# Kernel tuning notes

Measured on AMD Instinct MI355X. Metric: run time of the kernel, lower is better.

The kernel has to match this reference:

```python
import jax, jax.numpy as jnp
import numpy as np

H = W = 224
NUM_COLS = 1024          # static padded ring width (>= max pixels in any radial ring, ~703)
SHUFFLE_FRACTION = 0.5
BATCH = 128

def _build_maps():
    centre = (H // 2, W // 2)
    Y, X = np.ogrid[:H, :W]
    dist = np.round(np.sqrt((X - centre[0]) ** 2 + (Y - centre[1]) ** 2)).astype(np.int32)
    num_rows = int(dist[0, 0]) + 1
    ax2 = np.zeros_like(dist)
    for d in range(num_rows):
        m = dist == d
        ax2[m] = np.arange(m.sum(), dtype=np.int32)  # row-major order within each ring
    return dist, ax2, num_rows

_DIST_NP, _AX2_NP, NUM_ROWS = _build_maps()
DIST_FLAT = jnp.asarray(_DIST_NP.reshape(-1))  # (H*W,) radial bin of each pixel
AX2_FLAT = jnp.asarray(_AX2_NP.reshape(-1))    # (H*W,) index within its ring

def _process_one(img, mrand, prand):
    # img: (H, W); mrand: (H, W); prand: (NUM_ROWS, NUM_COLS)
    sel = mrand < SHUFFLE_FRACTION
    masked = jnp.where(sel, img, jnp.nan)
    # scatter selected pixels into polar bins (pixel -> (dist, ax2) is a bijection)
    polar = jnp.full((NUM_ROWS, NUM_COLS), jnp.nan, dtype=img.dtype)
    polar = polar.at[DIST_FLAT, AX2_FLAT].set(masked.reshape(-1))
    # random per-row permutation of columns
    perm = jnp.argsort(prand, axis=1)
    shuf = jnp.take_along_axis(polar, perm, axis=1)
    # compact the non-NaN shuffled values (in column order) back into the
    # originally-occupied columns (in ascending order) -- same as the TF
    # argsort(dists)/boolean-mask scatter, expressed with static shapes.
    src_order = jnp.argsort(jnp.isnan(shuf), axis=1)    # stable: non-NaN cols first
    vals = jnp.take_along_axis(shuf, src_order, axis=1)
    dst_order = jnp.argsort(jnp.isnan(polar), axis=1)   # stable: occupied cols first
    rows = jnp.arange(NUM_ROWS)[:, None]
    reinserted = shuf.at[rows, dst_order].set(vals)
    # gather each pixel's (possibly shuffled) value and write back selected pixels
    new_vals = reinserted[DIST_FLAT, AX2_FLAT].reshape(H, W)
    return jnp.where(sel, new_vals, img)

def setup_inputs() -> dict:
    key = jax.random.key(0)
    k1, k2, k3 = jax.random.split(key, 3)
    images = jax.random.normal(k1, (BATCH, H, W, 1), dtype=jnp.float32)
    mask_rand = jax.random.uniform(k2, (BATCH, H, W), dtype=jnp.float32)
    perm_rand = jax.random.uniform(k3, (BATCH, NUM_ROWS, NUM_COLS), dtype=jnp.float32)
    return {"images": images, "mask_rand": mask_rand, "perm_rand": perm_rand}

def reference(images, mask_rand, perm_rand):
    out = jax.vmap(_process_one)(images[..., 0], mask_rand, perm_rand)
    return out[..., None]
```

## Files before the change

kernel.cpp:

```cpp
#include <hip/hip_runtime.h>

#define IMG_H 224
#define IMG_W 224
#define HW (IMG_H * IMG_W)
#define HWB (HW / 8)
#define NUM_ROWS 159
#define NUM_COLS 1024
#define BATCH 128
#define OVF_CAP 4096
#define MAXC 12
#define NBUCK 512
#define NHWORDS (NBUCK / 2)
#define WPL (NHWORDS / 64)

__device__ __forceinline__ int isqrt_i(int v) {
    int u = (int)sqrtf((float)v);
    while (u > 0 && u * u > v) --u;
    while ((u + 1) * (u + 1) <= v) ++u;
    return u;
}

__device__ __forceinline__ void lds_fence() {
    asm volatile("s_waitcnt lgkmcnt(0)" ::: "memory");
}

__global__ __launch_bounds__(256) void build_rings(unsigned short* __restrict__ ring_pix,
                                                   int* __restrict__ ring_cnt,
                                                   int* __restrict__ ovf_cnt) {
    const int d = blockIdx.x;
    const int tid = threadIdx.x;
    __shared__ int scnt[256];
    if (d == 0 && tid == 0) ovf_cnt[0] = 0;

    int cnt = 0;
    int x0l = 0, x1l = -1, x0r = 0, x1r = -1;
    if (tid < IMG_H) {
        const int dy = tid - 112;
        const int Araw = (d == 0) ? 0 : (d * d - d + 1);
        int A = Araw - dy * dy;
        if (A < 0) A = 0;
        const int B = d * d + d - dy * dy;
        if (B >= 0) {
            const int hi = isqrt_i(B);
            int lo = isqrt_i(A);
            if (lo * lo < A) ++lo;
            if (lo <= hi) {
                if (lo == 0) {
                    x0l = 112 - min(hi, 112);
                    x1l = 112 + min(hi, 111);
                } else {
                    x0l = 112 - min(hi, 112);
                    x1l = 112 - lo;
                    x0r = 112 + lo;
                    x1r = 112 + min(hi, 111);
                }
                cnt = max(0, x1l - x0l + 1) + max(0, x1r - x0r + 1);
            }
        }
    }
    scnt[tid] = cnt;
    __syncthreads();
    for (int off = 1; off < 256; off <<= 1) {
        const int mine = scnt[tid];
        const int add = (tid >= off) ? scnt[tid - off] : 0;
        __syncthreads();
        scnt[tid] = mine + add;
        __syncthreads();
    }
    if (tid < IMG_H && cnt > 0) {
        int j = d * NUM_COLS + (scnt[tid] - cnt);
        const int rowbase = tid * IMG_W;
        for (int x = x0l; x <= x1l; ++x) ring_pix[j++] = (unsigned short)(rowbase + x);
        for (int x = x0r; x <= x1r; ++x) ring_pix[j++] = (unsigned short)(rowbase + x);
    }
    if (tid == 255) ring_cnt[d] = scnt[255];
}

__global__ __launch_bounds__(256) void copy_sel(const float4* __restrict__ img4,
                                                const float4* __restrict__ mask4,
                                                float4* __restrict__ out4,
                                                unsigned char* __restrict__ selb) {
    const int t = blockIdx.x * 256 + threadIdx.x;
    const float4 i0 = img4[2 * t];
    const float4 i1 = img4[2 * t + 1];
    const float4 m0 = mask4[2 * t];
    const float4 m1 = mask4[2 * t + 1];
    out4[2 * t] = i0;
    out4[2 * t + 1] = i1;
    const unsigned by = (m0.x < 0.5f ? 1u : 0u) | (m0.y < 0.5f ? 2u : 0u) |
                        (m0.z < 0.5f ? 4u : 0u) | (m0.w < 0.5f ? 8u : 0u) |
                        (m1.x < 0.5f ? 16u : 0u) | (m1.y < 0.5f ? 32u : 0u) |
                        (m1.z < 0.5f ? 64u : 0u) | (m1.w < 0.5f ? 128u : 0u);
    selb[t] = (unsigned char)by;
}

__device__ __forceinline__ void sort_run(unsigned long long* __restrict__ srt,
                                         int s, int e) {
    for (int i = s + 1; i < e; ++i) {
        const unsigned long long key = srt[i];
        int j = i - 1;
        while (j >= s && srt[j] > key) {
            srt[j + 1] = srt[j];
            --j;
        }
        srt[j + 1] = key;
    }
}

template <int CAP>
__device__ int gather_count_sort(
    int b, int d, int lane,
    const float* __restrict__ img, const unsigned char* __restrict__ selb,
    const float* __restrict__ prand, float* __restrict__ out,
    const unsigned short* __restrict__ ring_pix, int n,
    unsigned long long* __restrict__ srt, unsigned* __restrict__ hist,
    unsigned short* __restrict__ dstpix, float* __restrict__ vlds) {
    const float* imgb = img + (size_t)b * HW;
    const unsigned char* sbb = selb + (size_t)b * HWB;
    const float* prb = prand + ((size_t)b * NUM_ROWS + d) * NUM_COLS;
    float* outb = out + (size_t)b * HW;
    const unsigned long long ltmask = (1ull << lane) - 1ull;
    const unsigned short* rp = ring_pix + d * NUM_COLS;

#pragma unroll
    for (int t = 0; t < WPL; ++t) hist[t * 64 + lane] = 0;

    int p[MAXC];
    unsigned char sb[MAXC];
    unsigned kb[MAXC];
#pragma unroll
    for (int c = 0; c < MAXC; ++c) p[c] = rp[min(c * 64 + lane, n - 1)];
#pragma unroll
    for (int c = 0; c < MAXC; ++c) sb[c] = sbb[p[c] >> 3];
#pragma unroll
    for (int c = 0; c < MAXC; ++c) kb[c] = __float_as_uint(prb[min(c * 64 + lane, n - 1)]);

    unsigned selm = 0;
#pragma unroll
    for (int c = 0; c < MAXC; ++c) {
        const int i = c * 64 + lane;
        if ((i < n) && ((sb[c] >> (p[c] & 7)) & 1)) selm |= 1u << c;
    }

    float v[MAXC];
#pragma unroll
    for (int c = 0; c < MAXC; ++c)
        if ((selm >> c) & 1) v[c] = imgb[p[c]];

    lds_fence();

    int base = 0;
#pragma unroll
    for (int c = 0; c < MAXC; ++c) {
        const bool sel = (selm >> c) & 1;
        const unsigned long long ball = __ballot(sel);
        if (sel) {
            const int j = base + __popcll(ball & ltmask);
            if (j < CAP) dstpix[j] = (unsigned short)p[c];
            const int bk = (int)(__uint_as_float(kb[c]) * (float)NBUCK);
            atomicAdd(&hist[bk >> 1], 1u << ((bk & 1) * 16));
        }
        base += __popcll(ball);
    }
    const int base_static = base;
    for (int c0 = MAXC * 64; c0 < n; c0 += 64) {
        const int i = c0 + lane;
        bool sel = false;
        int pp = 0;
        unsigned kk = 0;
        if (i < n) {
            pp = rp[i];
            kk = __float_as_uint(prb[i]);
            sel = (sbb[pp >> 3] >> (pp & 7)) & 1;
        }
        const unsigned long long ball = __ballot(sel);
        if (sel) {
            const int j = base + __popcll(ball & ltmask);
            if (j < CAP) {
                dstpix[j] = (unsigned short)pp;
                vlds[j] = imgb[pp];
            }
            const int bk = (int)(__uint_as_float(kk) * (float)NBUCK);
            atomicAdd(&hist[bk >> 1], 1u << ((bk & 1) * 16));
        }
        base += __popcll(ball);
    }
    const int k = base;
    if (k > CAP) return k;
    if (k == 0) return 0;

    lds_fence();

    unsigned neww[WPL];
    unsigned run = 0;
#pragma unroll
    for (int t = 0; t < WPL; ++t) {
        const unsigned w = hist[lane * WPL + t];
        const unsigned c0 = w & 0xffffu;
        neww[t] = run | ((run + c0) << 16);
        run += c0 + (w >> 16);
    }
    const unsigned own = run;
#pragma unroll
    for (int off = 1; off < 64; off <<= 1) {
        const unsigned o = __shfl_up(run, off, 64);
        if (lane >= off) run += o;
    }
    const unsigned bx = run - own;
    const unsigned bxp = bx | (bx << 16);
    unsigned st[WPL];
#pragma unroll
    for (int t = 0; t < WPL; ++t) {
        st[t] = neww[t] + bxp;
        hist[lane * WPL + t] = st[t];
    }

    lds_fence();

    int jb = 0;
#pragma unroll
    for (int c = 0; c < MAXC; ++c) {
        const bool sel = (selm >> c) & 1;
        const unsigned long long ball = __ballot(sel);
        if (sel) {
            const int j = jb + __popcll(ball & ltmask);
            const int bk = (int)(__uint_as_float(kb[c]) * (float)NBUCK);
            const unsigned sh = (unsigned)((bk & 1) * 16);
            const unsigned old = atomicAdd(&hist[bk >> 1], 1u << sh);
            const int pos = (int)((old >> sh) & 0xffffu);
            srt[pos] = ((unsigned long long)kb[c] << 16) | (unsigned)j;
            vlds[j] = v[c];
        }
        jb += __popcll(ball);
    }
    int tb = base_static;
    for (int c0 = MAXC * 64; c0 < n; c0 += 64) {
        const int i = c0 + lane;
        bool sel = false;
        int pp = 0;
        unsigned kk = 0;
        if (i < n) {
            pp = rp[i];
            kk = __float_as_uint(prb[i]);
            sel = (sbb[pp >> 3] >> (pp & 7)) & 1;
        }
        const unsigned long long ball = __ballot(sel);
        if (sel) {
            const int j = tb + __popcll(ball & ltmask);
            const int bk = (int)(__uint_as_float(kk) * (float)NBUCK);
            const unsigned sh = (unsigned)((bk & 1) * 16);
            const unsigned old = atomicAdd(&hist[bk >> 1], 1u << sh);
            const int pos = (int)((old >> sh) & 0xffffu);
            srt[pos] = ((unsigned long long)kk << 16) | (unsigned)j;
        }
        tb += __popcll(ball);
    }

    lds_fence();

#pragma unroll
    for (int t = 0; t < WPL; ++t) {
        const unsigned wend = hist[lane * WPL + t];
        const unsigned ws0 = st[t];
        sort_run(srt, (int)(ws0 & 0xffffu), (int)(wend & 0xffffu));
        sort_run(srt, (int)(ws0 >> 16), (int)(wend >> 16));
    }

    lds_fence();

    const unsigned short* s16 = (const unsigned short*)srt;
#pragma unroll
    for (int e = 0; e < CAP / 64; ++e) {
        const int r = e * 64 + lane;
        if (r < k) {
            const int j = s16[4 * r];
            const float val = vlds[j];
            outb[dstpix[r]] = val;
        }
    }
    return k;
}

__global__ __launch_bounds__(256) void radial_shuffle(
    const float* __restrict__ img, const unsigned char* __restrict__ selb,
    const float* __restrict__ prand, float* __restrict__ out,
    const unsigned short* __restrict__ ring_pix, const int* __restrict__ ring_cnt,
    int* __restrict__ ovf_cnt, int* __restrict__ ovf_list) {
    const int tid = threadIdx.x;
    const int wid = tid >> 6;
    const int lane = tid & 63;
    const int xcd = blockIdx.x & 7;
    const int g = (blockIdx.x >> 3) * 4 + wid;
    const int b = xcd * (BATCH / 8) + g / NUM_ROWS;
    const int d = g % NUM_ROWS;
    const int n = ring_cnt[d];

    __shared__ unsigned long long srt_s[4][512];
    __shared__ unsigned hist_s[4][NHWORDS];
    __shared__ unsigned short dp_s[4][512];
    __shared__ float vl_s[4][512];

    const int k = gather_count_sort<512>(b, d, lane, img, selb, prand, out,
                                         ring_pix, n, srt_s[wid], hist_s[wid],
                                         dp_s[wid], vl_s[wid]);

    if (k > 512) {
        if (lane == 0) {
            const int idx = atomicAdd(ovf_cnt, 1);
            if (idx < OVF_CAP) ovf_list[idx] = b * NUM_ROWS + d;
        }
    }
}

__global__ __launch_bounds__(64) void overflow_sort(
    const float* __restrict__ img, const unsigned char* __restrict__ selb,
    const float* __restrict__ prand, float* __restrict__ out,
    const unsigned short* __restrict__ ring_pix, const int* __restrict__ ring_cnt,
    const int* __restrict__ ovf_cnt, const int* __restrict__ ovf_list) {
    __shared__ unsigned long long srt[1024];
    __shared__ unsigned hist[NHWORDS];
    __shared__ unsigned short dstpix[1024];
    __shared__ float vlds[1024];
    const int m = min(*ovf_cnt, OVF_CAP);
    const int lane = threadIdx.x;
    for (int t = blockIdx.x; t < m; t += gridDim.x) {
        const int bd = ovf_list[t];
        const int b = bd / NUM_ROWS;
        const int d = bd % NUM_ROWS;
        gather_count_sort<1024>(b, d, lane, img, selb, prand, out, ring_pix,
                                ring_cnt[d], srt, hist, dstpix, vlds);
        __syncthreads();
    }
}

extern "C" void kernel_launch(void* const* d_in, const int* in_sizes, int n_in,
                              void* d_out, int out_size, void* d_ws, size_t ws_size,
                              hipStream_t stream) {
    const float* img   = (const float*)d_in[0];
    const float* mask  = (const float*)d_in[1];
    const float* prand = (const float*)d_in[2];
    float* out = (float*)d_out;

    unsigned short* ring_pix = (unsigned short*)d_ws;
    int* ring_cnt = (int*)((char*)d_ws + NUM_ROWS * NUM_COLS * sizeof(unsigned short));
    int* ovf_cnt  = ring_cnt + NUM_ROWS;
    int* ovf_list = ovf_cnt + 1;
    unsigned char* selb = (unsigned char*)(ovf_list + OVF_CAP);

    hipLaunchKernelGGL(build_rings, dim3(NUM_ROWS), dim3(256), 0, stream,
                       ring_pix, ring_cnt, ovf_cnt);
    hipLaunchKernelGGL(copy_sel, dim3(BATCH * HW / 8 / 256), dim3(256), 0, stream,
                       (const float4*)img, (const float4*)mask, (float4*)out, selb);
    hipLaunchKernelGGL(radial_shuffle, dim3(BATCH * NUM_ROWS / 4), dim3(256), 0,
                       stream, img, selb, prand, out, ring_pix, ring_cnt,
                       ovf_cnt, ovf_list);
    hipLaunchKernelGGL(overflow_sort, dim3(32), dim3(64), 0, stream,
                       img, selb, prand, out, ring_pix, ring_cnt,
                       ovf_cnt, ovf_list);
}
```

Baseline: 201.0 us.

## Fuse pre-pass kernels, split sort keys, and scatter outputs directly per pixel

After: 198.4 us. Within noise of the previous version (-1.3%).

```diff
diff --git a/kernel.cpp b/kernel.cpp
--- a/kernel.cpp
+++ b/kernel.cpp
@@ -24,97 +24,101 @@
     asm volatile("s_waitcnt lgkmcnt(0)" ::: "memory");
 }
 
-__global__ __launch_bounds__(256) void build_rings(unsigned short* __restrict__ ring_pix,
-                                                   int* __restrict__ ring_cnt,
-                                                   int* __restrict__ ovf_cnt) {
-    const int d = blockIdx.x;
+__global__ __launch_bounds__(256) void pre_pass(
+    const float4* __restrict__ img4, const float4* __restrict__ mask4,
+    float4* __restrict__ out4, unsigned char* __restrict__ selb,
+    unsigned short* __restrict__ ring_pix, int* __restrict__ ring_cnt,
+    int* __restrict__ ovf_cnt) {
+    const int bid = blockIdx.x;
     const int tid = threadIdx.x;
     __shared__ int scnt[256];
-    if (d == 0 && tid == 0) ovf_cnt[0] = 0;
-
-    int cnt = 0;
-    int x0l = 0, x1l = -1, x0r = 0, x1r = -1;
-    if (tid < IMG_H) {
-        const int dy = tid - 112;
-        const int Araw = (d == 0) ? 0 : (d * d - d + 1);
-        int A = Araw - dy * dy;
-        if (A < 0) A = 0;
-        const int B = d * d + d - dy * dy;
-        if (B >= 0) {
-            const int hi = isqrt_i(B);
-            int lo = isqrt_i(A);
-            if (lo * lo < A) ++lo;
-            if (lo <= hi) {
-                if (lo == 0) {
-                    x0l = 112 - min(hi, 112);
-                    x1l = 112 + min(hi, 111);
-                } else {
-                    x0l = 112 - min(hi, 112);
-                    x1l = 112 - lo;
-                    x0r = 112 + lo;
-                    x1r = 112 + min(hi, 111);
+
+    if (bid < NUM_ROWS) {
+        const int d = bid;
+        if (d == 0 && tid == 0) ovf_cnt[0] = 0;
+        int cnt = 0;
+        int x0l = 0, x1l = -1, x0r = 0, x1r = -1;
+        if (tid < IMG_H) {
+            const int dy = tid - 112;
+            const int Araw = (d == 0) ? 0 : (d * d - d + 1);
+            int A = Araw - dy * dy;
+            if (A < 0) A = 0;
+            const int B = d * d + d - dy * dy;
+            if (B >= 0) {
+                const int hi = isqrt_i(B);
+                int lo = isqrt_i(A);
+                if (lo * lo < A) ++lo;
+                if (lo <= hi) {
+                    if (lo == 0) {
+                        x0l = 112 - min(hi, 112);
+                        x1l = 112 + min(hi, 111);
+                    } else {
+                        x0l = 112 - min(hi, 112);
+                        x1l = 112 - lo;
+                        x0r = 112 + lo;
+                        x1r = 112 + min(hi, 111);
+                    }
+                    cnt = max(0, x1l - x0l + 1) + max(0, x1r - x0r + 1);
                 }
-                cnt = max(0, x1l - x0l + 1) + max(0, x1r - x0r + 1);
             }
         }
-    }
-    scnt[tid] = cnt;
-    __syncthreads();
-    for (int off = 1; off < 256; off <<= 1) {
-        const int mine = scnt[tid];
-        const int add = (tid >= off) ? scnt[tid - off] : 0;
+        scnt[tid] = cnt;
         __syncthreads();
-        scnt[tid] = mine + add;
-        __syncthreads();
-    }
-    if (tid < IMG_H && cnt > 0) {
-        int j = d * NUM_COLS + (scnt[tid] - cnt);
-        const int rowbase = tid * IMG_W;
-        for (int x = x0l; x <= x1l; ++x) ring_pix[j++] = (unsigned short)(rowbase + x);
-        for (int x = x0r; x <= x1r; ++x) ring_pix[j++] = (unsigned short)(rowbase + x);
-    }
-    if (tid == 255) ring_cnt[d] = scnt[255];
-}
-
-__global__ __launch_bounds__(256) void copy_sel(const float4* __restrict__ img4,
-                                                const float4* __restrict__ mask4,
-                                                float4* __restrict__ out4,
-                                                unsigned char* __restrict__ selb) {
-    const int t = blockIdx.x * 256 + threadIdx.x;
-    const float4 i0 = img4[2 * t];
-    const float4 i1 = img4[2 * t + 1];
-    const float4 m0 = mask4[2 * t];
-    const float4 m1 = mask4[2 * t + 1];
-    out4[2 * t] = i0;
-    out4[2 * t + 1] = i1;
-    const unsigned by = (m0.x < 0.5f ? 1u : 0u) | (m0.y < 0.5f ? 2u : 0u) |
-                        (m0.z < 0.5f ? 4u : 0u) | (m0.w < 0.5f ? 8u : 0u) |
-                        (m1.x < 0.5f ? 16u : 0u) | (m1.y < 0.5f ? 32u : 0u) |
-                        (m1.z < 0.5f ? 64u : 0u) | (m1.w < 0.5f ? 128u : 0u);
-    selb[t] = (unsigned char)by;
-}
-
-__device__ __forceinline__ void sort_run(unsigned long long* __restrict__ srt,
-                                         int s, int e) {
+        for (int off = 1; off < 256; off <<= 1) {
+            const int mine = scnt[tid];
+            const int add = (tid >= off) ? scnt[tid - off] : 0;
+            __syncthreads();
+            scnt[tid] = mine + add;
+            __syncthreads();
+        }
+        if (tid < IMG_H && cnt > 0) {
+            int j = d * NUM_COLS + (scnt[tid] - cnt);
+            const int rowbase = tid * IMG_W;
+            for (int x = x0l; x <= x1l; ++x) ring_pix[j++] = (unsigned short)(rowbase + x);
+            for (int x = x0r; x <= x1r; ++x) ring_pix[j++] = (unsigned short)(rowbase + x);
+        }
+        if (tid == 255) ring_cnt[d] = scnt[255];
+    } else {
+        const int t = (bid - NUM_ROWS) * 256 + tid;
+        const float4 i0 = img4[2 * t];
+        const float4 i1 = img4[2 * t + 1];
+        const float4 m0 = mask4[2 * t];
+        const float4 m1 = mask4[2 * t + 1];
+        out4[2 * t] = i0;
+        out4[2 * t + 1] = i1;
+        const unsigned by = (m0.x < 0.5f ? 1u : 0u) | (m0.y < 0.5f ? 2u : 0u) |
+                            (m0.z < 0.5f ? 4u : 0u) | (m0.w < 0.5f ? 8u : 0u) |
+                            (m1.x < 0.5f ? 16u : 0u) | (m1.y < 0.5f ? 32u : 0u) |
+                            (m1.z < 0.5f ? 64u : 0u) | (m1.w < 0.5f ? 128u : 0u);
+        selb[t] = (unsigned char)by;
+    }
+}
+
+__device__ __forceinline__ void sort_run2(unsigned* __restrict__ k32,
+                                          unsigned short* __restrict__ j16,
+                                          int s, int e) {
     for (int i = s + 1; i < e; ++i) {
-        const unsigned long long key = srt[i];
-        int j = i - 1;
-        while (j >= s && srt[j] > key) {
-            srt[j + 1] = srt[j];
-            --j;
-        }
-        srt[j + 1] = key;
+        const unsigned key = k32[i];
+        const unsigned short jj = j16[i];
+        int q = i - 1;
+        while (q >= s && (k32[q] > key || (k32[q] == key && j16[q] > jj))) {
+            k32[q + 1] = k32[q];
+            j16[q + 1] = j16[q];
+            --q;
+        }
+        k32[q + 1] = key;
+        j16[q + 1] = jj;
     }
 }
 
 template <int CAP>
 __device__ int gather_count_sort(
-    int b, int d, int lane,
+    int b, int d, int lane, int n,
     const float* __restrict__ img, const unsigned char* __restrict__ selb,
     const float* __restrict__ prand, float* __restrict__ out,
-    const unsigned short* __restrict__ ring_pix, int n,
-    unsigned long long* __restrict__ srt, unsigned* __restrict__ hist,
-    unsigned short* __restrict__ dstpix, float* __restrict__ vlds) {
+    const unsigned short* __restrict__ ring_pix,
+    unsigned* __restrict__ srt32, unsigned short* __restrict__ srtj,
+    unsigned* __restrict__ hist, float* __restrict__ vlds) {
     const float* imgb = img + (size_t)b * HW;
     const unsigned char* sbb = selb + (size_t)b * HWB;
     const float* prb = prand + ((size_t)b * NUM_ROWS + d) * NUM_COLS;
@@ -129,39 +133,45 @@
     unsigned char sb[MAXC];
     unsigned kb[MAXC];
 #pragma unroll
-    for (int c = 0; c < MAXC; ++c) p[c] = rp[min(c * 64 + lane, n - 1)];
-#pragma unroll
-    for (int c = 0; c < MAXC; ++c) sb[c] = sbb[p[c] >> 3];
-#pragma unroll
-    for (int c = 0; c < MAXC; ++c) kb[c] = __float_as_uint(prb[min(c * 64 + lane, n - 1)]);
+    for (int c = 0; c < MAXC; ++c)
+        if (c * 64 < n) p[c] = rp[min(c * 64 + lane, n - 1)];
+#pragma unroll
+    for (int c = 0; c < MAXC; ++c)
+        if (c * 64 < n) sb[c] = sbb[p[c] >> 3];
+#pragma unroll
+    for (int c = 0; c < MAXC; ++c)
+        if (c * 64 < n) kb[c] = __float_as_uint(prb[c * 64 + lane]);
 
     unsigned selm = 0;
 #pragma unroll
-    for (int c = 0; c < MAXC; ++c) {
-        const int i = c * 64 + lane;
-        if ((i < n) && ((sb[c] >> (p[c] & 7)) & 1)) selm |= 1u << c;
-    }
+    for (int c = 0; c < MAXC; ++c)
+        if (c * 64 < n) {
+            if ((c * 64 + lane) < n && ((sb[c] >> (p[c] & 7)) & 1)) selm |= 1u << c;
+        }
 
     float v[MAXC];
 #pragma unroll
     for (int c = 0; c < MAXC; ++c)
-        if ((selm >> c) & 1) v[c] = imgb[p[c]];
-
-    lds_fence();
-
+        if (c * 64 < n) {
+            if ((selm >> c) & 1) v[c] = imgb[p[c]];
+        }
+
+    lds_fence();
+
+    int jc[MAXC];
     int base = 0;
 #pragma unroll
-    for (int c = 0; c < MAXC; ++c) {
-        const bool sel = (selm >> c) & 1;
-        const unsigned long long ball = __ballot(sel);
-        if (sel) {
-            const int j = base + __popcll(ball & ltmask);
-            if (j < CAP) dstpix[j] = (unsigned short)p[c];
-            const int bk = (int)(__uint_as_float(kb[c]) * (float)NBUCK);
-            atomicAdd(&hist[bk >> 1], 1u << ((bk & 1) * 16));
-        }
-        base += __popcll(ball);
-    }
+    for (int c = 0; c < MAXC; ++c)
+        if (c * 64 < n) {
+            const bool sel = (selm >> c) & 1;
+            const unsigned long long ball = __ballot(sel);
+            if (sel) {
+                jc[c] = base + __popcll(ball & ltmask);
+                const int bk = (int)(__uint_as_float(kb[c]) * (float)NBUCK);
+                atomicAdd(&hist[bk >> 1], 1u << ((bk & 1) * 16));
+            }
+            base += __popcll(ball);
+        }
     const int base_static = base;
     for (int c0 = MAXC * 64; c0 < n; c0 += 64) {
         const int i = c0 + lane;
@@ -176,10 +186,7 @@
         const unsigned long long ball = __ballot(sel);
         if (sel) {
             const int j = base + __popcll(ball & ltmask);
-            if (j < CAP) {
-                dstpix[j] = (unsigned short)pp;
-                vlds[j] = imgb[pp];
-            }
+            if (j < CAP) vlds[j] = imgb[pp];
             const int bk = (int)(__uint_as_float(kk) * (float)NBUCK);
             atomicAdd(&hist[bk >> 1], 1u << ((bk & 1) * 16));
         }
@@ -217,22 +224,19 @@
 
     lds_fence();
 
-    int jb = 0;
-#pragma unroll
-    for (int c = 0; c < MAXC; ++c) {
-        const bool sel = (selm >> c) & 1;
-        const unsigned long long ball = __ballot(sel);
-        if (sel) {
-            const int j = jb + __popcll(ball & ltmask);
-            const int bk = (int)(__uint_as_float(kb[c]) * (float)NBUCK);
-            const unsigned sh = (unsigned)((bk & 1) * 16);
-            const unsigned old = atomicAdd(&hist[bk >> 1], 1u << sh);
-            const int pos = (int)((old >> sh) & 0xffffu);
-            srt[pos] = ((unsigned long long)kb[c] << 16) | (unsigned)j;
-            vlds[j] = v[c];
-        }
-        jb += __popcll(ball);
-    }
+#pragma unroll
+    for (int c = 0; c < MAXC; ++c)
+        if (c * 64 < n) {
+            if ((selm >> c) & 1) {
+                const int bk = (int)(__uint_as_float(kb[c]) * (float)NBUCK);
+                const unsigned sh = (unsigned)((bk & 1) * 16);
+                const unsigned old = atomicAdd(&hist[bk >> 1], 1u << sh);
+                const int pos = (int)((old >> sh) & 0xffffu);
+                srt32[pos] = kb[c];
+                srtj[pos] = (unsigned short)jc[c];
+                vlds[jc[c]] = v[c];
+            }
+        }
     int tb = base_static;
     for (int c0 = MAXC * 64; c0 < n; c0 += 64) {
         const int i = c0 + lane;
@@ -251,7 +255,8 @@
             const unsigned sh = (unsigned)((bk & 1) * 16);
             const unsigned old = atomicAdd(&hist[bk >> 1], 1u << sh);
             const int pos = (int)((old >> sh) & 0xffffu);
-            srt[pos] = ((unsigned long long)kk << 16) | (unsigned)j;
+            srt32[pos] = kk;
+            srtj[pos] = (unsigned short)j;
         }
         tb += __popcll(ball);
     }
@@ -262,26 +267,41 @@
     for (int t = 0; t < WPL; ++t) {
         const unsigned wend = hist[lane * WPL + t];
         const unsigned ws0 = st[t];
-        sort_run(srt, (int)(ws0 & 0xffffu), (int)(wend & 0xffffu));
-        sort_run(srt, (int)(ws0 >> 16), (int)(wend >> 16));
-    }
-
-    lds_fence();
-
-    const unsigned short* s16 = (const unsigned short*)srt;
-#pragma unroll
-    for (int e = 0; e < CAP / 64; ++e) {
-        const int r = e * 64 + lane;
-        if (r < k) {
-            const int j = s16[4 * r];
-            const float val = vlds[j];
-            outb[dstpix[r]] = val;
-        }
+        sort_run2(srt32, srtj, (int)(ws0 & 0xffffu), (int)(wend & 0xffffu));
+        sort_run2(srt32, srtj, (int)(ws0 >> 16), (int)(wend >> 16));
+    }
+
+    lds_fence();
+
+#pragma unroll
+    for (int c = 0; c < MAXC; ++c)
+        if (c * 64 < n) {
+            if ((selm >> c) & 1) {
+                const int jp = srtj[jc[c]];
+                outb[p[c]] = vlds[jp];
+            }
+        }
+    tb = base_static;
+    for (int c0 = MAXC * 64; c0 < n; c0 += 64) {
+        const int i = c0 + lane;
+        bool sel = false;
+        int pp = 0;
+        if (i < n) {
+            pp = rp[i];
+            sel = (sbb[pp >> 3] >> (pp & 7)) & 1;
+        }
+        const unsigned long long ball = __ballot(sel);
+        if (sel) {
+            const int j = tb + __popcll(ball & ltmask);
+            const int jp = srtj[j];
+            outb[pp] = vlds[jp];
+        }
+        tb += __popcll(ball);
     }
     return k;
 }
 
-__global__ __launch_bounds__(256) void radial_shuffle(
+__global__ __launch_bounds__(256, 6) void radial_shuffle(
     const float* __restrict__ img, const unsigned char* __restrict__ selb,
     const float* __restrict__ prand, float* __restrict__ out,
     const unsigned short* __restrict__ ring_pix, const int* __restrict__ ring_cnt,
@@ -293,16 +313,16 @@
     const int g = (blockIdx.x >> 3) * 4 + wid;
     const int b = xcd * (BATCH / 8) + g / NUM_ROWS;
     const int d = g % NUM_ROWS;
-    const int n = ring_cnt[d];
-
-    __shared__ unsigned long long srt_s[4][512];
+    const int n = __builtin_amdgcn_readfirstlane(ring_cnt[d]);
+
+    __shared__ unsigned srt32_s[4][512];
+    __shared__ unsigned short srtj_s[4][512];
     __shared__ unsigned hist_s[4][NHWORDS];
-    __shared__ unsigned short dp_s[4][512];
     __shared__ float vl_s[4][512];
 
-    const int k = gather_count_sort<512>(b, d, lane, img, selb, prand, out,
-                                         ring_pix, n, srt_s[wid], hist_s[wid],
-                                         dp_s[wid], vl_s[wid]);
+    const int k = gather_count_sort<512>(b, d, lane, n, img, selb, prand, out,
+                                         ring_pix, srt32_s[wid], srtj_s[wid],
+                                         hist_s[wid], vl_s[wid]);
 
     if (k > 512) {
         if (lane == 0) {
@@ -317,9 +337,9 @@
     const float* __restrict__ prand, float* __restrict__ out,
     const unsigned short* __restrict__ ring_pix, const int* __restrict__ ring_cnt,
     const int* __restrict__ ovf_cnt, const int* __restrict__ ovf_list) {
-    __shared__ unsigned long long srt[1024];
+    __shared__ unsigned srt32[1024];
+    __shared__ unsigned short srtj[1024];
     __shared__ unsigned hist[NHWORDS];
-    __shared__ unsigned short dstpix[1024];
     __shared__ float vlds[1024];
     const int m = min(*ovf_cnt, OVF_CAP);
     const int lane = threadIdx.x;
@@ -327,8 +347,9 @@
         const int bd = ovf_list[t];
         const int b = bd / NUM_ROWS;
         const int d = bd % NUM_ROWS;
-        gather_count_sort<1024>(b, d, lane, img, selb, prand, out, ring_pix,
-                                ring_cnt[d], srt, hist, dstpix, vlds);
+        const int n = __builtin_amdgcn_readfirstlane(ring_cnt[d]);
+        gather_count_sort<1024>(b, d, lane, n, img, selb, prand, out, ring_pix,
+                                srt32, srtj, hist, vlds);
         __syncthreads();
     }
 }
@@ -347,10 +368,9 @@
     int* ovf_list = ovf_cnt + 1;
     unsigned char* selb = (unsigned char*)(ovf_list + OVF_CAP);
 
-    hipLaunchKernelGGL(build_rings, dim3(NUM_ROWS), dim3(256), 0, stream,
-                       ring_pix, ring_cnt, ovf_cnt);
-    hipLaunchKernelGGL(copy_sel, dim3(BATCH * HW / 8 / 256), dim3(256), 0, stream,
-                       (const float4*)img, (const float4*)mask, (float4*)out, selb);
+    hipLaunchKernelGGL(pre_pass, dim3(NUM_ROWS + BATCH * HW / 8 / 256), dim3(256),
+                       0, stream, (const float4*)img, (const float4*)mask,
+                       (float4*)out, selb, ring_pix, ring_cnt, ovf_cnt);
     hipLaunchKernelGGL(radial_shuffle, dim3(BATCH * NUM_ROWS / 4), dim3(256), 0,
                        stream, img, selb, prand, out, ring_pix, ring_cnt,
                        ovf_cnt, ovf_list);
```
